# Kernel tuning notes

Hardware: AMD Instinct MI355X
Metric: run time of the kernel (lower is better)

The kernel has to match this reference:

```python
import jax, jax.numpy as jnp
import numpy as np

NHEADS = 16
KVHEADS = 4
HEAD_DIM = 128  # emb_kq_per_head == emb_v_per_head
ROPE_THETA = 10000.0


def _rotary(x, cos, sin):
    # x: [B, S, H, D]; half-split rotation
    x1, x2 = jnp.split(x, 2, axis=-1)
    rot = jnp.concatenate([-x2, x1], axis=-1)
    return x * cos + rot * sin


def setup_inputs() -> dict:
    key = jax.random.key(0)
    k1, k2, k3 = jax.random.split(key, 3)
    B, S, E = 2, 2048, 2048
    qkv_out = NHEADS * HEAD_DIM + 2 * KVHEADS * HEAD_DIM  # 3072
    return {
        "x": jax.random.normal(k1, (B, S, E), dtype=jnp.float32),
        "w_qkv": jax.random.normal(k2, (E, qkv_out), dtype=jnp.float32) * 0.02,
        "w_dense": jax.random.normal(k3, (NHEADS * HEAD_DIM, E), dtype=jnp.float32) * 0.02,
    }


def reference(x, w_qkv, w_dense):
    B, S, E = x.shape
    D = HEAD_DIM
    # fused QKV projection (use_bias=False), then split per FusedQKV.splits
    qkv = x @ w_qkv  # [B, S, 3072]
    q, k, v = jnp.split(qkv, [NHEADS * D, NHEADS * D + KVHEADS * D], axis=-1)
    q = q.reshape(B, S, NHEADS, D)
    k = k.reshape(B, S, KVHEADS, D)
    v = v.reshape(B, S, KVHEADS, D)

    # rotary position encoding, positions = arange(S)
    pos = jnp.arange(S, dtype=jnp.float32)
    inv_freq = 1.0 / (ROPE_THETA ** (jnp.arange(0, D, 2, dtype=jnp.float32) / D))
    ang = pos[:, None] * inv_freq[None, :]                 # [S, D/2]
    ang = jnp.concatenate([ang, ang], axis=-1)             # [S, D]
    cos = jnp.cos(ang)[None, :, None, :]                   # [1, S, 1, D]
    sin = jnp.sin(ang)[None, :, None, :]
    q = _rotary(q, cos, sin)
    k = _rotary(k, cos, sin)

    # GQA: expand kv heads to query heads
    rep = NHEADS // KVHEADS
    k = jnp.repeat(k, rep, axis=2)  # [B, S, NHEADS, D]
    v = jnp.repeat(v, rep, axis=2)

    scale = 1.0 / jnp.sqrt(jnp.asarray(D, dtype=x.dtype))
    scores = jnp.einsum("bqhd,bkhd->bhqk", q, k) * scale   # [B, H, S, S]
    causal = jnp.tril(jnp.ones((S, S), dtype=bool))
    scores = jnp.where(causal[None, None], scores, jnp.finfo(scores.dtype).min)
    probs = jax.nn.softmax(scores, axis=-1)
    attn = jnp.einsum("bhqk,bkhd->bqhd", probs, v)         # [B, S, H, D]
    attn = attn.reshape(B, S, NHEADS * D)
    return attn @ w_dense                                  # [B, S, E]
```

## Files before the change

### kernel.cpp

```cpp
#include <hip/hip_runtime.h>
#include <type_traits>


typedef __attribute__((ext_vector_type(8))) short short8;
typedef __attribute__((ext_vector_type(4))) float floatx4;
typedef __attribute__((ext_vector_type(4))) unsigned short ushort4v;
typedef __attribute__((ext_vector_type(4))) unsigned int uint4v;

constexpr int NH    = 16;
constexpr int NKV   = 4;
constexpr int HD    = 128;
constexpr int SEQ   = 2048;
constexpr int EMB   = 2048;
constexpr int NBATCH = 2;
constexpr int MROWS = NBATCH * SEQ;
constexpr int NQKV  = (NH + 2 * NKV) * HD;

__device__ __forceinline__ unsigned short f2b(float f) {
  union { float f; unsigned u; } v; v.f = f;
  unsigned u = v.u + 0x7FFFu + ((v.u >> 16) & 1u);
  return (unsigned short)(u >> 16);
}
__device__ __forceinline__ float b2f(unsigned short h) {
  union { unsigned u; float f; } v; v.u = (unsigned)h << 16;
  return v.f;
}

__device__ __forceinline__ void gload_lds16(const unsigned short* g,
                                            unsigned short* lds) {
  __builtin_amdgcn_global_load_lds(
      (const __attribute__((address_space(1))) unsigned int*)g,
      (__attribute__((address_space(3))) unsigned int*)lds, 16, 0, 0);
}

__global__ void cvt_f32_bf16(const float* __restrict__ in,
                             unsigned short* __restrict__ out, int n) {
  int i = (blockIdx.x * 256 + threadIdx.x) * 4;
  if (i + 3 < n) {
    floatx4 v = *(const floatx4*)(in + i);
    ushort4v o = { f2b(v[0]), f2b(v[1]), f2b(v[2]), f2b(v[3]) };
    *(ushort4v*)(out + i) = o;
  }
}

__global__ void transpose_cvt_dual(const float* __restrict__ wqkv,
                                   unsigned short* __restrict__ oqkv,
                                   const float* __restrict__ wd,
                                   unsigned short* __restrict__ od) {
  const int z = blockIdx.z;
  const float* in = z ? wd : wqkv;
  unsigned short* out = z ? od : oqkv;
  const int R = EMB;
  const int C = z ? EMB : NQKV;
  int c0 = blockIdx.x * 32, r0 = blockIdx.y * 32;
  if (c0 >= C) return;
  __shared__ float t[32][33];
  int tx = threadIdx.x & 31, ty = threadIdx.x >> 5;
#pragma unroll
  for (int i = 0; i < 32; i += 8)
    t[ty + i][tx] = in[(long)(r0 + ty + i) * C + (c0 + tx)];
  __syncthreads();
#pragma unroll
  for (int i = 0; i < 32; i += 8)
    out[(long)(c0 + ty + i) * R + (r0 + tx)] = f2b(t[tx][ty + i]);
}

__global__ void rope_kernel(unsigned short* __restrict__ Qb,
                            unsigned short* __restrict__ Kb, float qscale) {
  int idx = blockIdx.x * 256 + threadIdx.x;
  int i = idx & 63;
  int s = (idx >> 6) & (SEQ - 1);
  int bh = idx >> 17;
  unsigned short* p;
  float scale;
  if (bh < NBATCH * NH) { p = Qb + ((long)bh * SEQ + s) * HD; scale = qscale; }
  else { p = Kb + ((long)(bh - NBATCH * NH) * SEQ + s) * HD; scale = 1.0f; }
  float e = -(float)i * (2.0f * 13.287712379549449f / 128.0f);
  float ang = (float)s * exp2f(e);
  float sn, c;
  sincosf(ang, &sn, &c);
  float x1 = b2f(p[i]), x2 = b2f(p[i + 64]);
  p[i]      = f2b((x1 * c - x2 * sn) * scale);
  p[i + 64] = f2b((x2 * c + x1 * sn) * scale);
}

constexpr int BM = 128, BN = 128, BK = 64;

template <int MODE>
__global__ __launch_bounds__(256, 3) void gemm_bt(
    const unsigned short* __restrict__ A,
    const unsigned short* __restrict__ BT,
    int Mdim, int Ndim, int Kdim,
    float* __restrict__ outF,
    unsigned short* __restrict__ Qb,
    unsigned short* __restrict__ Kb,
    unsigned short* __restrict__ Vt) {
  __shared__ __align__(16) unsigned short smem[BM * BK + BN * BK];
  unsigned short (*As)[BK] = (unsigned short (*)[BK])smem;
  unsigned short (*Bs)[BK] = (unsigned short (*)[BK])(smem + BM * BK);
  const int tid = threadIdx.x;
  const int bm = blockIdx.y * BM;
  const int bn = blockIdx.x * BN;
  const int wave = tid >> 6, lane = tid & 63;
  const int l = lane & 15, q = lane >> 4;
  const int l7 = l & 7;
  const int wm = (wave >> 1) * 64, wn = (wave & 1) * 64;

  floatx4 acc[4][4] = {};

  const int srow = lane >> 3;
  const int scol = ((lane & 7) ^ srow) * 8;
  const unsigned short* Arow = A + (long)bm * Kdim;
  const unsigned short* Brow = BT + (long)bn * Kdim;

  for (int k0 = 0; k0 < Kdim; k0 += BK) {
#pragma unroll
    for (int i = 0; i < 4; ++i) {
      const int r0 = wave * 32 + i * 8;
      gload_lds16(Arow + (long)(r0 + srow) * Kdim + k0 + scol, &As[r0][0]);
      gload_lds16(Brow + (long)(r0 + srow) * Kdim + k0 + scol, &Bs[r0][0]);
    }
    __syncthreads();
#pragma unroll
    for (int kk = 0; kk < 2; ++kk) {
      short8 af[4], bfr[4];
#pragma unroll
      for (int mi = 0; mi < 4; ++mi)
        af[mi] = *(const short8*)&As[wm + mi * 16 + l][((kk * 4 + q) ^ l7) * 8];
#pragma unroll
      for (int ni = 0; ni < 4; ++ni)
        bfr[ni] = *(const short8*)&Bs[wn + ni * 16 + l][((kk * 4 + q) ^ l7) * 8];
#pragma unroll
      for (int mi = 0; mi < 4; ++mi)
#pragma unroll
        for (int ni = 0; ni < 4; ++ni)
          acc[mi][ni] = __builtin_amdgcn_mfma_f32_16x16x32_bf16(
              af[mi], bfr[ni], acc[mi][ni], 0, 0, 0);
    }
    __syncthreads();
  }

  if constexpr (MODE == 1) {
#pragma unroll
    for (int mi = 0; mi < 4; ++mi) {
      const int rowbase = bm + wm + mi * 16 + q * 4;
#pragma unroll
      for (int ni = 0; ni < 4; ++ni) {
        const int col = bn + wn + ni * 16 + l;
#pragma unroll
        for (int r = 0; r < 4; ++r)
          outF[(long)(rowbase + r) * Ndim + col] = acc[mi][ni][r];
      }
    }
  } else if (bn >= (NH + NKV) * HD) {
    const int hh = (bn - (NH + NKV) * HD) >> 7;
#pragma unroll
    for (int mi = 0; mi < 4; ++mi) {
      const int m0 = bm + wm + mi * 16 + q * 4;
      const int bb = m0 >> 11, s = m0 & (SEQ - 1);
      const int s6 = s & 63;
      const int p6 = (s6 & 32) | ((s6 & 12) << 1) | ((s6 & 16) >> 2);
      const int sp = (s & ~63) | p6;
      unsigned short* vtb = Vt + ((long)(bb * NKV + hh)) * HD * SEQ;
#pragma unroll
      for (int ni = 0; ni < 4; ++ni) {
        const int d = wn + ni * 16 + l;
        ushort4v pv = { f2b(acc[mi][ni][0]), f2b(acc[mi][ni][1]),
                        f2b(acc[mi][ni][2]), f2b(acc[mi][ni][3]) };
        *(ushort4v*)(vtb + (long)d * SEQ + sp) = pv;
      }
    }
  } else {
    unsigned short (*Ct)[128] = (unsigned short (*)[128])smem;
#pragma unroll
    for (int mi = 0; mi < 4; ++mi)
#pragma unroll
      for (int ni = 0; ni < 4; ++ni)
#pragma unroll
        for (int r = 0; r < 4; ++r) {
          const int row = wm + mi * 16 + q * 4 + r;
          const int col = wn + ni * 16 + l;
          const int cs = ((((col >> 3) ^ row) & 7) | (col & 64 ? 8 : 0)) * 8 + (col & 7);
          Ct[row][cs] = f2b(acc[mi][ni][r]);
        }
    __syncthreads();
    const int row = tid >> 1, g = tid & 1;
    const int m = bm + row, bb = m >> 11, s = m & (SEQ - 1);
    unsigned short* dst;
    if (bn < NH * HD)
      dst = Qb + (((long)(bb * NH + (bn >> 7))) * SEQ + s) * HD;
    else
      dst = Kb + (((long)(bb * NKV + ((bn - NH * HD) >> 7))) * SEQ + s) * HD;
#pragma unroll
    for (int i = 0; i < 8; ++i) {
      const int blk = (g * 8) + (i ^ (row & 7));
      *(short8*)(dst + g * 64 + i * 8) = *(const short8*)&Ct[row][blk * 8];
    }
  }
}

__global__ __launch_bounds__(256, 2) void attn_kernel(
    const unsigned short* __restrict__ Q,
    const unsigned short* __restrict__ K,
    const unsigned short* __restrict__ VT,
    unsigned short* __restrict__ attn) {
  const int h = blockIdx.y, b = blockIdx.z;
  const int t = b ? (15 - (int)blockIdx.x) : (int)blockIdx.x;
  const int kvh = h >> 2;
  const int tid = threadIdx.x;
  const int wave = tid >> 6, lane = tid & 63;
  const int l = lane & 15, q = lane >> 4;
  const int l7 = l & 7;
  const int wq = wave * 32;

  const unsigned short* Kh  = K  + ((long)(b * NKV + kvh)) * SEQ * HD;
  const unsigned short* VTh = VT + ((long)(b * NKV + kvh)) * HD * SEQ;

  __shared__ __align__(16) unsigned short smem[2 * 64 * 128 + 2 * 128 * 64];
  unsigned short (*Ks)[64 * 128]  = (unsigned short (*)[64 * 128])smem;
  unsigned short (*VTs)[128 * 64] = (unsigned short (*)[128 * 64])(smem + 2 * 64 * 128);

  int koff[4], voff[4];
  {
    const int k_rl = lane >> 4, k_bp = lane & 15;
    const int v_rl = lane >> 3, v_bp = lane & 7;
#pragma unroll
    for (int j = 0; j < 4; ++j) {
      const int rk = (wave * 4 + j) * 4 + k_rl;
      koff[j] = rk * HD + (k_bp ^ (rk & 15)) * 8;
      const int rv = (wave * 4 + j) * 8 + v_rl;
      voff[j] = rv * SEQ + (v_bp ^ (rv & 7)) * 8;
    }
  }

  short8 onesf;
#pragma unroll
  for (int i = 0; i < 8; ++i) onesf[i] = (short)0x3F80;

  auto stage = [&](int c, int buf) {
    const unsigned short* kc = Kh + c * (64 * HD);
    const unsigned short* vc = VTh + c * 64;
#pragma unroll
    for (int j = 0; j < 4; ++j)
      gload_lds16(kc + koff[j], &Ks[buf][(wave * 4 + j) * 4 * 128]);
#pragma unroll
    for (int j = 0; j < 4; ++j)
      gload_lds16(vc + voff[j], &VTs[buf][(wave * 4 + j) * 8 * 64]);
  };

  const unsigned short* Qh = Q + (((long)(b * NH + h)) * SEQ + t * 128) * HD;
  short8 qf[2][4];
#pragma unroll
  for (int mh = 0; mh < 2; ++mh)
#pragma unroll
    for (int kk = 0; kk < 4; ++kk)
      qf[mh][kk] = *(const short8*)(Qh + (long)(wq + mh * 16 + l) * HD + kk * 32 + q * 8);

  floatx4 o[2][9] = {};

  auto chunk_body = [&](auto masked, int cur, int kv0) {
    constexpr bool MASKED = decltype(masked)::value;
    floatx4 sf[2][4] = {};
#pragma unroll
    for (int kk = 0; kk < 4; ++kk) {
      short8 kf[4];
#pragma unroll
      for (int ni = 0; ni < 4; ++ni)
        kf[ni] = *(const short8*)&Ks[cur][(ni * 16 + l) * 128 + (((kk * 4 + q) ^ l) * 8)];
#pragma unroll
      for (int mh = 0; mh < 2; ++mh)
#pragma unroll
        for (int ni = 0; ni < 4; ++ni)
          sf[mh][ni] = __builtin_amdgcn_mfma_f32_16x16x32_bf16(
              kf[ni], qf[mh][kk], sf[mh][ni], 0, 0, 0);
    }
    short8 pf[2][2];
#pragma unroll
    for (int mh = 0; mh < 2; ++mh) {
      const int qrow = t * 128 + wq + mh * 16 + l;
      unsigned u[8];
#pragma unroll
      for (int ni = 0; ni < 4; ++ni) {
        if constexpr (MASKED) {
#pragma unroll
          for (int r = 0; r < 4; ++r)
            if (kv0 + ni * 16 + q * 4 + r > qrow) sf[mh][ni][r] = -3e38f;
        }
        float e0 = exp2f(sf[mh][ni][0]);
        float e1 = exp2f(sf[mh][ni][1]);
        float e2 = exp2f(sf[mh][ni][2]);
        float e3 = exp2f(sf[mh][ni][3]);
        asm("v_cvt_pk_bf16_f32 %0, %1, %2" : "=v"(u[ni * 2]) : "v"(e0), "v"(e1));
        asm("v_cvt_pk_bf16_f32 %0, %1, %2" : "=v"(u[ni * 2 + 1]) : "v"(e2), "v"(e3));
      }
      union { uint4v v; short8 s; } a0, a1;
      a0.v = (uint4v){u[0], u[1], u[2], u[3]};
      a1.v = (uint4v){u[4], u[5], u[6], u[7]};
      pf[mh][0] = a0.s;
      pf[mh][1] = a1.s;
    }
#pragma unroll
    for (int c2 = 0; c2 < 2; ++c2) {
      const int pb = ((c2 * 4 + q) ^ l7) * 8;
#pragma unroll
      for (int di = 0; di < 8; ++di) {
        short8 vf = *(const short8*)&VTs[cur][(di * 16 + l) * 64 + pb];
        o[0][di] = __builtin_amdgcn_mfma_f32_16x16x32_bf16(pf[0][c2], vf, o[0][di], 0, 0, 0);
        o[1][di] = __builtin_amdgcn_mfma_f32_16x16x32_bf16(pf[1][c2], vf, o[1][di], 0, 0, 0);
      }
      o[0][8] = __builtin_amdgcn_mfma_f32_16x16x32_bf16(pf[0][c2], onesf, o[0][8], 0, 0, 0);
      o[1][8] = __builtin_amdgcn_mfma_f32_16x16x32_bf16(pf[1][c2], onesf, o[1][8], 0, 0, 0);
    }
  };

  const int nc = 2 * t + 2;
  stage(0, 0);
  __syncthreads();

  int c = 0;
#pragma unroll 1
  for (; c < nc - 2; ++c) {
    stage(c + 1, (c & 1) ^ 1);
    chunk_body(std::false_type{}, c & 1, c * 64);
    __syncthreads();
  }
  stage(c + 1, (c & 1) ^ 1);
  chunk_body(std::true_type{}, c & 1, c * 64);
  __syncthreads();
  ++c;
  chunk_body(std::true_type{}, c & 1, c * 64);
  __syncthreads();

  unsigned short (*Ob)[136] = (unsigned short (*)[136])smem;
#pragma unroll
  for (int mh = 0; mh < 2; ++mh)
#pragma unroll
    for (int r = 0; r < 4; ++r) {
      const float inv = 1.0f / o[mh][8][r];
#pragma unroll
      for (int di = 0; di < 8; ++di)
        Ob[wq + mh * 16 + q * 4 + r][di * 16 + l] = f2b(o[mh][di][r] * inv);
    }
  __syncthreads();
  {
    const int row = tid >> 1, g = (tid & 1) * 64;
    const int s = t * 128 + row;
    unsigned short* dst = attn + ((long)(b * SEQ + s)) * (NH * HD) + h * HD + g;
#pragma unroll
    for (int j = 0; j < 8; ++j)
      *(short8*)(dst + j * 8) = *(const short8*)&Ob[row][g + j * 8];
  }
}

extern "C" void kernel_launch(void* const* d_in, const int* in_sizes, int n_in,
                              void* d_out, int out_size, void* d_ws, size_t ws_size,
                              hipStream_t stream) {
  const float* x       = (const float*)d_in[0];
  const float* w_qkv   = (const float*)d_in[1];
  const float* w_dense = (const float*)d_in[2];
  float* out = (float*)d_out;

  char* ws = (char*)d_ws;
  const size_t MB = 1024 * 1024;
  unsigned short* xb    = (unsigned short*)(ws);
  unsigned short* wqkvT = (unsigned short*)(ws + 16 * MB);
  unsigned short* wdT   = (unsigned short*)(ws + 28 * MB);
  unsigned short* Qb    = (unsigned short*)(ws + 36 * MB);
  unsigned short* Kb    = (unsigned short*)(ws + 52 * MB);
  unsigned short* VTb   = (unsigned short*)(ws + 56 * MB);
  unsigned short* attn  = xb;

  const float qscale = 0.08838834764831845f * 1.4426950408889634f;

  cvt_f32_bf16<<<(MROWS * EMB) / (256 * 4), 256, 0, stream>>>(x, xb, MROWS * EMB);
  transpose_cvt_dual<<<dim3(NQKV / 32, EMB / 32, 2), 256, 0, stream>>>(
      w_qkv, wqkvT, w_dense, wdT);

  gemm_bt<0><<<dim3(NQKV / BN, MROWS / BM), 256, 0, stream>>>(
      xb, wqkvT, MROWS, NQKV, EMB, nullptr, Qb, Kb, VTb);

  rope_kernel<<<(NBATCH * (NH + NKV) * SEQ * 64) / 256, 256, 0, stream>>>(Qb, Kb, qscale);

  attn_kernel<<<dim3(16, NH, NBATCH), 256, 0, stream>>>(Qb, Kb, VTb, attn);

  gemm_bt<1><<<dim3(EMB / BN, MROWS / BM), 256, 0, stream>>>(
      attn, wdT, MROWS, EMB, NH * HD, out, nullptr, nullptr, nullptr);
}
```

Measured before the change: 283.0 us.

## Rewrite GEMM as 256x256 tile, 8-wave, double-buffered pipelined kernel

Replaces the 128x128 single-buffered GEMM with a 256x256 tile run by 512 threads. It uses 128KB of dynamic LDS split into two buffers, and a hand-scheduled loop that interleaves global-to-LDS loads for the next k-tile with MFMA sections, using explicit waitcnt, barriers and setprio. The goal is to hide memory latency and raise data reuse per block. In exchange the grid is smaller: 192 blocks for the QKV GEMM and 128 for the dense GEMM, which may underfill the 256 CUs. The hand-written wait counts are fragile.

```diff
diff --git a/kernel.cpp b/kernel.cpp
--- a/kernel.cpp
+++ b/kernel.cpp
@@ -84,10 +84,38 @@
   p[i + 64] = f2b((x2 * c + x1 * sn) * scale);
 }
 
-constexpr int BM = 128, BN = 128, BK = 64;
+
+#define G_BARRIER __builtin_amdgcn_s_barrier()
+#define G_LGKM0 asm volatile("s_waitcnt lgkmcnt(0)" ::: "memory")
+#define G_LGKM8 asm volatile("s_waitcnt lgkmcnt(8)" ::: "memory")
+#define G_VM(N) asm volatile("s_waitcnt vmcnt(" #N ")" ::: "memory")
+
+#define READ_A(BUF, MH)                                                        \
+  _Pragma("unroll") for (int kk = 0; kk < 2; ++kk)                             \
+  _Pragma("unroll") for (int mi = 0; mi < 4; ++mi)                             \
+    af[kk][mi] = *(const short8*)&sm[(BUF)*16384 +                             \
+        ((MH)*128 + wr64 + mi*16 + l)*64 + kb[kk]];
+
+#define READ_B(BUF, NH)                                                        \
+  _Pragma("unroll") for (int kk = 0; kk < 2; ++kk)                             \
+  _Pragma("unroll") for (int ni = 0; ni < 2; ++ni)                             \
+    bf[NH][kk][ni] = *(const short8*)&sm[32768 + (BUF)*16384 +                 \
+        ((NH)*128 + wc32 + ni*16 + l)*64 + kb[kk]];
+
+#define MFMA_SECT(MH, NH)                                                      \
+  G_BARRIER;                                                                   \
+  G_LGKM0;                                                                     \
+  __builtin_amdgcn_s_setprio(1);                                               \
+  _Pragma("unroll") for (int kk = 0; kk < 2; ++kk)                             \
+  _Pragma("unroll") for (int mi = 0; mi < 4; ++mi)                             \
+  _Pragma("unroll") for (int ni = 0; ni < 2; ++ni)                             \
+    acc[MH][mi][NH][ni] = __builtin_amdgcn_mfma_f32_16x16x32_bf16(             \
+        af[kk][mi], bf[NH][kk][ni], acc[MH][mi][NH][ni], 0, 0, 0);             \
+  __builtin_amdgcn_s_setprio(0);                                               \
+  G_BARRIER
 
 template <int MODE>
-__global__ __launch_bounds__(256, 3) void gemm_bt(
+__global__ __launch_bounds__(512, 2) void gemm_bt(
     const unsigned short* __restrict__ A,
     const unsigned short* __restrict__ BT,
     int Mdim, int Ndim, int Kdim,
@@ -95,106 +123,140 @@
     unsigned short* __restrict__ Qb,
     unsigned short* __restrict__ Kb,
     unsigned short* __restrict__ Vt) {
-  __shared__ __align__(16) unsigned short smem[BM * BK + BN * BK];
-  unsigned short (*As)[BK] = (unsigned short (*)[BK])smem;
-  unsigned short (*Bs)[BK] = (unsigned short (*)[BK])(smem + BM * BK);
+  extern __shared__ __align__(16) unsigned short sm[];
   const int tid = threadIdx.x;
-  const int bm = blockIdx.y * BM;
-  const int bn = blockIdx.x * BN;
   const int wave = tid >> 6, lane = tid & 63;
   const int l = lane & 15, q = lane >> 4;
   const int l7 = l & 7;
-  const int wm = (wave >> 1) * 64, wn = (wave & 1) * 64;
-
-  floatx4 acc[4][4] = {};
-
+  const int wr = wave >> 2, wc = wave & 3;
+  const int wr64 = wr * 64, wc32 = wc * 32;
+  const int bm = blockIdx.y * 256;
+  const int bn = blockIdx.x * 256;
   const int srow = lane >> 3;
   const int scol = ((lane & 7) ^ srow) * 8;
-  const unsigned short* Arow = A + (long)bm * Kdim;
-  const unsigned short* Brow = BT + (long)bn * Kdim;
-
-  for (int k0 = 0; k0 < Kdim; k0 += BK) {
-#pragma unroll
-    for (int i = 0; i < 4; ++i) {
-      const int r0 = wave * 32 + i * 8;
-      gload_lds16(Arow + (long)(r0 + srow) * Kdim + k0 + scol, &As[r0][0]);
-      gload_lds16(Brow + (long)(r0 + srow) * Kdim + k0 + scol, &Bs[r0][0]);
-    }
-    __syncthreads();
-#pragma unroll
-    for (int kk = 0; kk < 2; ++kk) {
-      short8 af[4], bfr[4];
+  const int kb[2] = { (q ^ l7) * 8, ((4 + q) ^ l7) * 8 };
+
+  floatx4 acc[2][4][2][2] = {};
+  short8 af[2][4];
+  short8 bf[2][2][2];
+
+  auto stA = [&](int buf, int h, int kt) {
+    const unsigned short* s0 = A +
+        (long)(bm + (wave >> 2) * 128 + h * 64 + (wave & 3) * 16 + srow) * Kdim +
+        kt * 64 + scol;
+    unsigned short* d0 = &sm[buf * 16384 + (h * 128 + wave * 16) * 64];
+    gload_lds16(s0, d0);
+    gload_lds16(s0 + 8L * Kdim, d0 + 8 * 64);
+  };
+  auto stB = [&](int buf, int h, int kt) {
+    const unsigned short* s0 = BT +
+        (long)(bn + (wave >> 1) * 64 + h * 32 + (wave & 1) * 16 + srow) * Kdim +
+        kt * 64 + scol;
+    unsigned short* d0 = &sm[32768 + buf * 16384 + (h * 128 + wave * 16) * 64];
+    gload_lds16(s0, d0);
+    gload_lds16(s0 + 8L * Kdim, d0 + 8 * 64);
+  };
+
+  stA(0, 0, 0); stB(0, 0, 0); stB(0, 1, 0); stA(0, 1, 0);
+  G_VM(4);
+  stA(1, 0, 1); stB(1, 1, 1); stA(1, 1, 1);
+  G_VM(6);
+  G_BARRIER;
+
+  const int niter = Kdim / 128 - 1;
+#pragma unroll 1
+  for (int i = 0; i < niter; ++i) {
+    const int kt = 2 * i;
+    READ_A(0, 0) READ_B(0, 0) stB(1, 0, kt + 1); G_LGKM8; MFMA_SECT(0, 0);
+    READ_B(0, 1) stA(0, 0, kt + 2); MFMA_SECT(0, 1);
+    READ_A(0, 1) stB(0, 1, kt + 2); MFMA_SECT(1, 1);
+    stA(0, 1, kt + 2); G_VM(6); MFMA_SECT(1, 0);
+    READ_A(1, 0) READ_B(1, 0) stB(0, 0, kt + 2); G_LGKM8; MFMA_SECT(0, 0);
+    READ_B(1, 1) stA(1, 0, kt + 3); MFMA_SECT(0, 1);
+    READ_A(1, 1) stB(1, 1, kt + 3); MFMA_SECT(1, 1);
+    stA(1, 1, kt + 3); G_VM(6); MFMA_SECT(1, 0);
+  }
+  {
+    const int kt = 2 * niter;
+    READ_A(0, 0) READ_B(0, 0) stB(1, 0, kt + 1); G_LGKM8; MFMA_SECT(0, 0);
+    READ_B(0, 1) G_VM(4); MFMA_SECT(0, 1);
+    READ_A(0, 1) G_VM(2); MFMA_SECT(1, 1);
+    G_VM(0); MFMA_SECT(1, 0);
+    READ_A(1, 0) READ_B(1, 0) G_LGKM8; MFMA_SECT(0, 0);
+    READ_B(1, 1) MFMA_SECT(0, 1);
+    READ_A(1, 1) MFMA_SECT(1, 1);
+    MFMA_SECT(1, 0);
+  }
+
+  if constexpr (MODE == 1) {
+#pragma unroll
+    for (int mh = 0; mh < 2; ++mh)
+#pragma unroll
+      for (int mi = 0; mi < 4; ++mi) {
+        const int rowb = bm + wr * 128 + mh * 64 + mi * 16 + q * 4;
+#pragma unroll
+        for (int nh = 0; nh < 2; ++nh)
+#pragma unroll
+          for (int ni = 0; ni < 2; ++ni) {
+            const int col = bn + wc * 64 + nh * 32 + ni * 16 + l;
+#pragma unroll
+            for (int r = 0; r < 4; ++r)
+              outF[(long)(rowb + r) * Ndim + col] = acc[mh][mi][nh][ni][r];
+          }
+      }
+  } else if (bn >= (NH + NKV) * HD) {
+    const int hh0 = (bn - (NH + NKV) * HD) >> 7;
+#pragma unroll
+    for (int mh = 0; mh < 2; ++mh)
+#pragma unroll
+      for (int mi = 0; mi < 4; ++mi) {
+        const int m0 = bm + wr * 128 + mh * 64 + mi * 16 + q * 4;
+        const int bb = m0 >> 11, s = m0 & (SEQ - 1);
+        const int s6 = s & 63;
+        const int p6 = (s6 & 32) | ((s6 & 12) << 1) | ((s6 & 16) >> 2);
+        const long spb = (long)((s & ~63) | p6);
+#pragma unroll
+        for (int nh = 0; nh < 2; ++nh)
+#pragma unroll
+          for (int ni = 0; ni < 2; ++ni) {
+            const int col = wc * 64 + nh * 32 + ni * 16 + l;
+            const int hh = hh0 + (col >> 7), d = col & 127;
+            unsigned short* vtb = Vt + ((long)(bb * NKV + hh)) * HD * SEQ;
+            ushort4v pv = { f2b(acc[mh][mi][nh][ni][0]), f2b(acc[mh][mi][nh][ni][1]),
+                            f2b(acc[mh][mi][nh][ni][2]), f2b(acc[mh][mi][nh][ni][3]) };
+            *(ushort4v*)(vtb + (long)d * SEQ + spb) = pv;
+          }
+      }
+  } else {
+    unsigned short* Ct = sm;
+#pragma unroll
+    for (int mh = 0; mh < 2; ++mh)
 #pragma unroll
       for (int mi = 0; mi < 4; ++mi)
-        af[mi] = *(const short8*)&As[wm + mi * 16 + l][((kk * 4 + q) ^ l7) * 8];
-#pragma unroll
-      for (int ni = 0; ni < 4; ++ni)
-        bfr[ni] = *(const short8*)&Bs[wn + ni * 16 + l][((kk * 4 + q) ^ l7) * 8];
-#pragma unroll
-      for (int mi = 0; mi < 4; ++mi)
-#pragma unroll
-        for (int ni = 0; ni < 4; ++ni)
-          acc[mi][ni] = __builtin_amdgcn_mfma_f32_16x16x32_bf16(
-              af[mi], bfr[ni], acc[mi][ni], 0, 0, 0);
-    }
-    __syncthreads();
-  }
-
-  if constexpr (MODE == 1) {
-#pragma unroll
-    for (int mi = 0; mi < 4; ++mi) {
-      const int rowbase = bm + wm + mi * 16 + q * 4;
-#pragma unroll
-      for (int ni = 0; ni < 4; ++ni) {
-        const int col = bn + wn + ni * 16 + l;
-#pragma unroll
-        for (int r = 0; r < 4; ++r)
-          outF[(long)(rowbase + r) * Ndim + col] = acc[mi][ni][r];
-      }
-    }
-  } else if (bn >= (NH + NKV) * HD) {
-    const int hh = (bn - (NH + NKV) * HD) >> 7;
-#pragma unroll
-    for (int mi = 0; mi < 4; ++mi) {
-      const int m0 = bm + wm + mi * 16 + q * 4;
-      const int bb = m0 >> 11, s = m0 & (SEQ - 1);
-      const int s6 = s & 63;
-      const int p6 = (s6 & 32) | ((s6 & 12) << 1) | ((s6 & 16) >> 2);
-      const int sp = (s & ~63) | p6;
-      unsigned short* vtb = Vt + ((long)(bb * NKV + hh)) * HD * SEQ;
-#pragma unroll
-      for (int ni = 0; ni < 4; ++ni) {
-        const int d = wn + ni * 16 + l;
-        ushort4v pv = { f2b(acc[mi][ni][0]), f2b(acc[mi][ni][1]),
-                        f2b(acc[mi][ni][2]), f2b(acc[mi][ni][3]) };
-        *(ushort4v*)(vtb + (long)d * SEQ + sp) = pv;
-      }
-    }
-  } else {
-    unsigned short (*Ct)[128] = (unsigned short (*)[128])smem;
-#pragma unroll
-    for (int mi = 0; mi < 4; ++mi)
-#pragma unroll
-      for (int ni = 0; ni < 4; ++ni)
-#pragma unroll
-        for (int r = 0; r < 4; ++r) {
-          const int row = wm + mi * 16 + q * 4 + r;
-          const int col = wn + ni * 16 + l;
-          const int cs = ((((col >> 3) ^ row) & 7) | (col & 64 ? 8 : 0)) * 8 + (col & 7);
-          Ct[row][cs] = f2b(acc[mi][ni][r]);
-        }
+#pragma unroll
+        for (int nh = 0; nh < 2; ++nh)
+#pragma unroll
+          for (int ni = 0; ni < 2; ++ni)
+#pragma unroll
+            for (int r = 0; r < 4; ++r) {
+              const int row = wr * 128 + mh * 64 + mi * 16 + q * 4 + r;
+              const int col = wc * 64 + nh * 32 + ni * 16 + l;
+              const int blk = col >> 3;
+              const int cs = ((blk & 24) | ((blk ^ row) & 7)) * 8 + (col & 7);
+              Ct[row * 256 + cs] = f2b(acc[mh][mi][nh][ni][r]);
+            }
     __syncthreads();
     const int row = tid >> 1, g = tid & 1;
     const int m = bm + row, bb = m >> 11, s = m & (SEQ - 1);
+    const int hg = (bn >> 7) + g;
     unsigned short* dst;
-    if (bn < NH * HD)
-      dst = Qb + (((long)(bb * NH + (bn >> 7))) * SEQ + s) * HD;
-    else
-      dst = Kb + (((long)(bb * NKV + ((bn - NH * HD) >> 7))) * SEQ + s) * HD;
-#pragma unroll
-    for (int i = 0; i < 8; ++i) {
-      const int blk = (g * 8) + (i ^ (row & 7));
-      *(short8*)(dst + g * 64 + i * 8) = *(const short8*)&Ct[row][blk * 8];
+    if (hg < NH) dst = Qb + (((long)(bb * NH + hg)) * SEQ + s) * HD;
+    else         dst = Kb + (((long)(bb * NKV + (hg - NH))) * SEQ + s) * HD;
+#pragma unroll
+    for (int i = 0; i < 16; ++i) {
+      const int blk = g * 16 + i;
+      const int pb = (blk & 24) | ((blk ^ row) & 7);
+      *(short8*)(dst + i * 8) = *(const short8*)&Ct[row * 256 + pb * 8];
     }
   }
 }
@@ -370,19 +432,28 @@
   unsigned short* VTb   = (unsigned short*)(ws + 56 * MB);
   unsigned short* attn  = xb;
 
+  static bool attr_set = false;
+  if (!attr_set) {
+    (void)hipFuncSetAttribute(reinterpret_cast<const void*>(&gemm_bt<0>),
+                              hipFuncAttributeMaxDynamicSharedMemorySize, 131072);
+    (void)hipFuncSetAttribute(reinterpret_cast<const void*>(&gemm_bt<1>),
+                              hipFuncAttributeMaxDynamicSharedMemorySize, 131072);
+    attr_set = true;
+  }
+
   const float qscale = 0.08838834764831845f * 1.4426950408889634f;
 
   cvt_f32_bf16<<<(MROWS * EMB) / (256 * 4), 256, 0, stream>>>(x, xb, MROWS * EMB);
   transpose_cvt_dual<<<dim3(NQKV / 32, EMB / 32, 2), 256, 0, stream>>>(
       w_qkv, wqkvT, w_dense, wdT);
 
-  gemm_bt<0><<<dim3(NQKV / BN, MROWS / BM), 256, 0, stream>>>(
+  gemm_bt<0><<<dim3(NQKV / 256, MROWS / 256), 512, 131072, stream>>>(
       xb, wqkvT, MROWS, NQKV, EMB, nullptr, Qb, Kb, VTb);
 
   rope_kernel<<<(NBATCH * (NH + NKV) * SEQ * 64) / 256, 256, 0, stream>>>(Qb, Kb, qscale);
 
   attn_kernel<<<dim3(16, NH, NBATCH), 256, 0, stream>>>(Qb, Kb, VTb, attn);
 
-  gemm_bt<1><<<dim3(EMB / BN, MROWS / BM), 256, 0, stream>>>(
+  gemm_bt<1><<<dim3(EMB / 256, MROWS / 256), 512, 131072, stream>>>(
       attn, wdT, MROWS, EMB, NH * HD, out, nullptr, nullptr, nullptr);
 }
```

Measured after the change: 292.3 us. 3.3% more time.

## Fuse RoPE into QKV GEMM epilogue and narrow dense GEMM tile

Applied to the files above, without the earlier changes.

Removes the standalone rotary kernel by applying RoPE and the query scale inside the QKV GEMM's Q/K epilogue, reading both rotation halves from the shared-memory staging tile. This drops a full read-modify-write pass over Q and K in global memory plus one kernel launch. Separately, the output-projection GEMM now uses a 128x64 tile with a higher occupancy target, doubling its block count to better fill the GPU. The epilogue gains per-element sincos work, which may add latency to the GEMM tail.

```diff
diff --git a/kernel.cpp b/kernel.cpp
--- a/kernel.cpp
+++ b/kernel.cpp
@@ -65,48 +65,32 @@
     out[(long)(c0 + ty + i) * R + (r0 + tx)] = f2b(t[tx][ty + i]);
 }
 
-__global__ void rope_kernel(unsigned short* __restrict__ Qb,
-                            unsigned short* __restrict__ Kb, float qscale) {
-  int idx = blockIdx.x * 256 + threadIdx.x;
-  int i = idx & 63;
-  int s = (idx >> 6) & (SEQ - 1);
-  int bh = idx >> 17;
-  unsigned short* p;
-  float scale;
-  if (bh < NBATCH * NH) { p = Qb + ((long)bh * SEQ + s) * HD; scale = qscale; }
-  else { p = Kb + ((long)(bh - NBATCH * NH) * SEQ + s) * HD; scale = 1.0f; }
-  float e = -(float)i * (2.0f * 13.287712379549449f / 128.0f);
-  float ang = (float)s * exp2f(e);
-  float sn, c;
-  sincosf(ang, &sn, &c);
-  float x1 = b2f(p[i]), x2 = b2f(p[i + 64]);
-  p[i]      = f2b((x1 * c - x2 * sn) * scale);
-  p[i + 64] = f2b((x2 * c + x1 * sn) * scale);
-}
-
-constexpr int BM = 128, BN = 128, BK = 64;
+constexpr int BM = 128, BK = 64;
 
 template <int MODE>
-__global__ __launch_bounds__(256, 3) void gemm_bt(
+__global__ __launch_bounds__(256, MODE == 1 ? 4 : 3) void gemm_bt(
     const unsigned short* __restrict__ A,
     const unsigned short* __restrict__ BT,
     int Mdim, int Ndim, int Kdim,
     float* __restrict__ outF,
     unsigned short* __restrict__ Qb,
     unsigned short* __restrict__ Kb,
-    unsigned short* __restrict__ Vt) {
-  __shared__ __align__(16) unsigned short smem[BM * BK + BN * BK];
+    unsigned short* __restrict__ Vt,
+    float qscale) {
+  constexpr int TBN = (MODE == 1) ? 64 : 128;
+  constexpr int NI  = TBN / 32;
+  __shared__ __align__(16) unsigned short smem[BM * BK + TBN * BK];
   unsigned short (*As)[BK] = (unsigned short (*)[BK])smem;
   unsigned short (*Bs)[BK] = (unsigned short (*)[BK])(smem + BM * BK);
   const int tid = threadIdx.x;
   const int bm = blockIdx.y * BM;
-  const int bn = blockIdx.x * BN;
+  const int bn = blockIdx.x * TBN;
   const int wave = tid >> 6, lane = tid & 63;
   const int l = lane & 15, q = lane >> 4;
   const int l7 = l & 7;
-  const int wm = (wave >> 1) * 64, wn = (wave & 1) * 64;
-
-  floatx4 acc[4][4] = {};
+  const int wm = (wave >> 1) * 64, wn = (wave & 1) * (TBN / 2);
+
+  floatx4 acc[4][NI] = {};
 
   const int srow = lane >> 3;
   const int scol = ((lane & 7) ^ srow) * 8;
@@ -118,22 +102,26 @@
     for (int i = 0; i < 4; ++i) {
       const int r0 = wave * 32 + i * 8;
       gload_lds16(Arow + (long)(r0 + srow) * Kdim + k0 + scol, &As[r0][0]);
+    }
+#pragma unroll
+    for (int i = 0; i < TBN / 32; ++i) {
+      const int r0 = wave * (TBN / 4) + i * 8;
       gload_lds16(Brow + (long)(r0 + srow) * Kdim + k0 + scol, &Bs[r0][0]);
     }
     __syncthreads();
 #pragma unroll
     for (int kk = 0; kk < 2; ++kk) {
-      short8 af[4], bfr[4];
+      short8 af[4], bfr[NI];
 #pragma unroll
       for (int mi = 0; mi < 4; ++mi)
         af[mi] = *(const short8*)&As[wm + mi * 16 + l][((kk * 4 + q) ^ l7) * 8];
 #pragma unroll
-      for (int ni = 0; ni < 4; ++ni)
+      for (int ni = 0; ni < NI; ++ni)
         bfr[ni] = *(const short8*)&Bs[wn + ni * 16 + l][((kk * 4 + q) ^ l7) * 8];
 #pragma unroll
       for (int mi = 0; mi < 4; ++mi)
 #pragma unroll
-        for (int ni = 0; ni < 4; ++ni)
+        for (int ni = 0; ni < NI; ++ni)
           acc[mi][ni] = __builtin_amdgcn_mfma_f32_16x16x32_bf16(
               af[mi], bfr[ni], acc[mi][ni], 0, 0, 0);
     }
@@ -145,7 +133,7 @@
     for (int mi = 0; mi < 4; ++mi) {
       const int rowbase = bm + wm + mi * 16 + q * 4;
 #pragma unroll
-      for (int ni = 0; ni < 4; ++ni) {
+      for (int ni = 0; ni < NI; ++ni) {
         const int col = bn + wn + ni * 16 + l;
 #pragma unroll
         for (int r = 0; r < 4; ++r)
@@ -163,7 +151,7 @@
       const int sp = (s & ~63) | p6;
       unsigned short* vtb = Vt + ((long)(bb * NKV + hh)) * HD * SEQ;
 #pragma unroll
-      for (int ni = 0; ni < 4; ++ni) {
+      for (int ni = 0; ni < NI; ++ni) {
         const int d = wn + ni * 16 + l;
         ushort4v pv = { f2b(acc[mi][ni][0]), f2b(acc[mi][ni][1]),
                         f2b(acc[mi][ni][2]), f2b(acc[mi][ni][3]) };
@@ -175,7 +163,7 @@
 #pragma unroll
     for (int mi = 0; mi < 4; ++mi)
 #pragma unroll
-      for (int ni = 0; ni < 4; ++ni)
+      for (int ni = 0; ni < NI; ++ni)
 #pragma unroll
         for (int r = 0; r < 4; ++r) {
           const int row = wm + mi * 16 + q * 4 + r;
@@ -186,15 +174,35 @@
     __syncthreads();
     const int row = tid >> 1, g = tid & 1;
     const int m = bm + row, bb = m >> 11, s = m & (SEQ - 1);
+    const bool isQ = (bn < NH * HD);
     unsigned short* dst;
-    if (bn < NH * HD)
-      dst = Qb + (((long)(bb * NH + (bn >> 7))) * SEQ + s) * HD;
-    else
-      dst = Kb + (((long)(bb * NKV + ((bn - NH * HD) >> 7))) * SEQ + s) * HD;
+    if (isQ) dst = Qb + (((long)(bb * NH + (bn >> 7))) * SEQ + s) * HD;
+    else     dst = Kb + (((long)(bb * NKV + ((bn - NH * HD) >> 7))) * SEQ + s) * HD;
+    const float scale = isQ ? qscale : 1.0f;
+    const float sf = (float)s;
 #pragma unroll
     for (int i = 0; i < 8; ++i) {
-      const int blk = (g * 8) + (i ^ (row & 7));
-      *(short8*)(dst + g * 64 + i * 8) = *(const short8*)&Ct[row][blk * 8];
+      const int lbo = g * 8 + i;
+      const int lbx = (g ^ 1) * 8 + i;
+      const int pbo = (lbo & 8) | ((lbo ^ row) & 7);
+      const int pbx = (lbx & 8) | ((lbx ^ row) & 7);
+      short8 xo = *(const short8*)&Ct[row][pbo * 8];
+      short8 xx = *(const short8*)&Ct[row][pbx * 8];
+      short8 outv;
+#pragma unroll
+      for (int j2 = 0; j2 < 8; ++j2) {
+        const int j = i * 8 + j2;
+        const float e = -(float)j * (2.0f * 13.287712379549449f / 128.0f);
+        const float ang = sf * exp2f(e);
+        float sn, cs_;
+        sincosf(ang, &sn, &cs_);
+        const float xown = b2f((unsigned short)xo[j2]);
+        const float xoth = b2f((unsigned short)xx[j2]);
+        const float rr = g ? (xown * cs_ + xoth * sn)
+                           : (xown * cs_ - xoth * sn);
+        outv[j2] = (short)f2b(rr * scale);
+      }
+      *(short8*)(dst + g * 64 + i * 8) = outv;
     }
   }
 }
@@ -376,13 +384,11 @@
   transpose_cvt_dual<<<dim3(NQKV / 32, EMB / 32, 2), 256, 0, stream>>>(
       w_qkv, wqkvT, w_dense, wdT);
 
-  gemm_bt<0><<<dim3(NQKV / BN, MROWS / BM), 256, 0, stream>>>(
-      xb, wqkvT, MROWS, NQKV, EMB, nullptr, Qb, Kb, VTb);
-
-  rope_kernel<<<(NBATCH * (NH + NKV) * SEQ * 64) / 256, 256, 0, stream>>>(Qb, Kb, qscale);
+  gemm_bt<0><<<dim3(NQKV / 128, MROWS / BM), 256, 0, stream>>>(
+      xb, wqkvT, MROWS, NQKV, EMB, nullptr, Qb, Kb, VTb, qscale);
 
   attn_kernel<<<dim3(16, NH, NBATCH), 256, 0, stream>>>(Qb, Kb, VTb, attn);
 
-  gemm_bt<1><<<dim3(EMB / BN, MROWS / BM), 256, 0, stream>>>(
-      attn, wdT, MROWS, EMB, NH * HD, out, nullptr, nullptr, nullptr);
-}
+  gemm_bt<1><<<dim3(EMB / 64, MROWS / BM), 256, 0, stream>>>(
+      attn, wdT, MROWS, EMB, NH * HD, out, nullptr, nullptr, nullptr, 0.0f);
+}
```

Result: no change. 282.1 us (-0.3%).
